# Performance work log

Hardware: AMD Instinct MI355X
Metric: run time of the kernel (lower is better)

## Reference

```python
import jax, jax.numpy as jnp
import numpy as np

A = 9  # len(scales) * len(ratios) anchor templates
DN = ('NHWC', 'HWIO', 'NHWC')


def _conv(x, w, b):
    y = jax.lax.conv_general_dilated(x, w, window_strides=(1, 1), padding='SAME',
                                     dimension_numbers=DN)
    return y + b


def setup_inputs() -> dict:
    key = jax.random.key(0)
    ks = jax.random.split(key, 9)
    s = 0.02  # weight init scale
    x = jax.random.normal(ks[0], (4, 128, 128, 512), jnp.float32)
    W1 = jax.random.normal(ks[1], (3, 3, 512, 256), jnp.float32) * s
    b1 = jnp.zeros((256,), jnp.float32)
    W2 = jax.random.normal(ks[2], (3, 3, 256, 256), jnp.float32) * s
    b2 = jnp.zeros((256,), jnp.float32)
    Wr = jax.random.normal(ks[3], (1, 1, 256, 4 * A), jnp.float32) * s
    br = jnp.zeros((4 * A,), jnp.float32)
    Wc = jax.random.normal(ks[4], (1, 1, 256, 2 * A), jnp.float32) * s
    bc = jnp.zeros((2 * A,), jnp.float32)
    return {'x': x, 'W1': W1, 'b1': b1, 'W2': W2, 'b2': b2,
            'Wr': Wr, 'br': br, 'Wc': Wc, 'bc': bc}


def reference(x, W1, b1, W2, b2, Wr, br, Wc, bc):
    h = jax.nn.relu(_conv(x, W1, b1))
    h = jax.nn.relu(_conv(h, W2, b2))
    B, H, W = h.shape[0], h.shape[1], h.shape[2]
    reg = _conv(h, Wr, br).reshape(B, H, W, A, 4)            # (B,H,W,A,4)
    cls = _conv(h, Wc, bc).reshape(B, H, W, A, 2)            # (B,H,W,A,2)
    cls = jax.nn.softmax(cls, axis=4)
    return jnp.concatenate((cls, reg), axis=4)               # (B,H,W,A,6)
```

## Files before the change

### kernel.cpp

```cpp
#include <hip/hip_runtime.h>


typedef float f32x4  __attribute__((ext_vector_type(4)));
typedef float f32x16 __attribute__((ext_vector_type(16)));
typedef short bf16x8 __attribute__((ext_vector_type(8)));

union U16x8 { uint4 v; unsigned short s[8]; };

__device__ __forceinline__ unsigned short f2bf(float f) {
  union { float f; unsigned int u; } v; v.f = f;
  unsigned int r = v.u + 0x7FFFu + ((v.u >> 16) & 1u);
  return (unsigned short)(r >> 16);
}

__global__ __launch_bounds__(256) void transpose_cvt(
    const float* __restrict__ src, unsigned short* __restrict__ dst,
    int K, int N) {
  __shared__ float t[32][33];
  const int tx = threadIdx.x, ty = threadIdx.y;
  const int k0 = blockIdx.x * 32, n0 = blockIdx.y * 32;
  const float* s = src + (size_t)blockIdx.z * K * N;
  unsigned short* d = dst + (size_t)blockIdx.z * N * K;
#pragma unroll
  for (int r = 0; r < 32; r += 8) {
    int k = k0 + ty + r, n = n0 + tx;
    t[ty + r][tx] = (k < K && n < N) ? s[(size_t)k * N + n] : 0.f;
  }
  __syncthreads();
#pragma unroll
  for (int r = 0; r < 32; r += 8) {
    int n = n0 + ty + r, k = k0 + tx;
    if (n < N && k < K) d[(size_t)n * K + k] = f2bf(t[tx][ty + r]);
  }
}

__global__ __launch_bounds__(256) void convert_x(
    const float* __restrict__ x, unsigned short* __restrict__ xp) {
  int idx = blockIdx.x * 256 + threadIdx.x;
  int g = idx & 63;
  int cell = idx >> 6;
  int xpix = cell % 130;
  int t = cell / 130;
  int ypix = t % 130;
  int b = t / 130;
  U16x8 u;
  if (xpix == 0 || xpix == 129 || ypix == 0 || ypix == 129) {
    u.v = make_uint4(0u, 0u, 0u, 0u);
  } else {
    const float* sp = x + ((size_t)((b * 128 + ypix - 1) * 128) + (xpix - 1)) * 512 + g * 8;
    float4 a = *(const float4*)sp;
    float4 c = *(const float4*)(sp + 4);
    u.s[0] = f2bf(a.x); u.s[1] = f2bf(a.y); u.s[2] = f2bf(a.z); u.s[3] = f2bf(a.w);
    u.s[4] = f2bf(c.x); u.s[5] = f2bf(c.y); u.s[6] = f2bf(c.z); u.s[7] = f2bf(c.w);
  }
  *(uint4*)(xp + (size_t)cell * 512 + g * 8) = u.v;
}

__global__ __launch_bounds__(256) void zero_h1_borders(unsigned short* __restrict__ h1p) {
  int idx = blockIdx.x * 256 + threadIdx.x;
  int g = idx & 31;
  int cell = idx >> 5;
  int xpix = cell % 130;
  int t = cell / 130;
  int ypix = t % 130;
  if (xpix == 0 || xpix == 129 || ypix == 0 || ypix == 129)
    *(uint4*)(h1p + (size_t)cell * 256 + g * 8) = make_uint4(0u, 0u, 0u, 0u);
}

template<int CIN, int MODE>
__global__ __launch_bounds__(256) void conv3x3(
    const unsigned short* __restrict__ Ap,
    const unsigned short* __restrict__ WT,
    const float* __restrict__ bias,
    unsigned short* __restrict__ out) {
  __shared__ __align__(16) unsigned short As[130][72];
  __shared__ __align__(16) unsigned short Bs[3][128][72];
  const int tid  = threadIdx.x;
  const int wave = tid >> 6, lane = tid & 63;
  const int wm = wave >> 1, wn = wave & 1;
  const int l31 = lane & 31, hi = lane >> 5;
  const int b = blockIdx.x >> 7, y = blockIdx.x & 127;
  const int nbase = blockIdx.y * 128;

  f32x16 acc[2][2] = {};

  for (int dy = 0; dy < 3; ++dy) {
    const unsigned short* Arow = Ap + ((size_t)(b * 130 + y + dy) * 130) * CIN;
    const unsigned short* Btap = WT + ((size_t)(dy * 3) * 256 + nbase) * CIN;
    for (int ci0 = 0; ci0 < CIN; ci0 += 64) {
      for (int s = tid; s < 1040; s += 256) {
        int row = s >> 3, seg = s & 7;
        *(uint4*)&As[row][seg * 8] =
            *(const uint4*)(Arow + (size_t)row * CIN + ci0 + seg * 8);
      }
#pragma unroll
      for (int t = 0; t < 12; ++t) {
        int s = t * 256 + tid;
        int dx = s >> 10, r = (s >> 3) & 127, seg = s & 7;
        *(uint4*)&Bs[dx][r][seg * 8] =
            *(const uint4*)(Btap + ((size_t)dx * 256 + r) * CIN + ci0 + seg * 8);
      }
      __syncthreads();
#pragma unroll
      for (int dx = 0; dx < 3; ++dx) {
#pragma unroll
        for (int ks = 0; ks < 4; ++ks) {
          bf16x8 af[2], bfr[2];
#pragma unroll
          for (int i = 0; i < 2; ++i)
            af[i] = *(const bf16x8*)&As[wm * 64 + i * 32 + l31 + dx][ks * 16 + hi * 8];
#pragma unroll
          for (int j = 0; j < 2; ++j)
            bfr[j] = *(const bf16x8*)&Bs[dx][wn * 64 + j * 32 + l31][ks * 16 + hi * 8];
#pragma unroll
          for (int i = 0; i < 2; ++i)
#pragma unroll
            for (int j = 0; j < 2; ++j)
              acc[i][j] = __builtin_amdgcn_mfma_f32_32x32x16_bf16(af[i], bfr[j], acc[i][j], 0, 0, 0);
        }
      }
      __syncthreads();
    }
  }

#pragma unroll
  for (int i = 0; i < 2; ++i) {
#pragma unroll
    for (int j = 0; j < 2; ++j) {
      int n = nbase + wn * 64 + j * 32 + l31;
      float bb = bias[n];
#pragma unroll
      for (int reg = 0; reg < 16; ++reg) {
        int m = wm * 64 + i * 32 + (reg & 3) + 8 * (reg >> 2) + 4 * hi;
        float v = fmaxf(acc[i][j][reg] + bb, 0.f);
        size_t off;
        if (MODE == 0)
          off = ((size_t)(b * 130 + y + 1) * 130 + (m + 1)) * 256 + n;
        else
          off = ((size_t)((b * 128 + y) * 128 + m)) * 256 + n;
        out[off] = f2bf(v);
      }
    }
  }
}

__global__ __launch_bounds__(256) void heads_kernel(
    const unsigned short* __restrict__ h2,
    const unsigned short* __restrict__ WhT,
    const float* __restrict__ br, const float* __restrict__ bc,
    float* __restrict__ out) {
  __shared__ __align__(16) unsigned short As[64][264];
  const int tid = threadIdx.x;
  const int wave = tid >> 6, lane = tid & 63;
  const int quad = lane >> 4, l16 = lane & 15;
  const int pix0 = blockIdx.x * 64;
#pragma unroll
  for (int r = 0; r < 8; ++r) {
    int s = r * 256 + tid;
    int row = s >> 5, seg = s & 31;
    *(uint4*)&As[row][seg * 8] =
        *(const uint4*)(h2 + (size_t)(pix0 + row) * 256 + seg * 8);
  }
  __syncthreads();
  f32x4 acc[4] = {};
#pragma unroll
  for (int ks = 0; ks < 8; ++ks) {
    bf16x8 af = *(const bf16x8*)&As[wave * 16 + l16][ks * 32 + quad * 8];
#pragma unroll
    for (int j = 0; j < 4; ++j) {
      bf16x8 bfr = *(const bf16x8*)(WhT + (size_t)(j * 16 + l16) * 256 + ks * 32 + quad * 8);
      acc[j] = __builtin_amdgcn_mfma_f32_16x16x32_bf16(af, bfr, acc[j], 0, 0, 0);
    }
  }
#pragma unroll
  for (int j = 0; j < 4; ++j) {
    int n = j * 16 + l16;
    float bias = 0.f;
    if (n < 18) bias = bc[n];
    else if (n < 54) bias = br[n - 18];
#pragma unroll
    for (int r = 0; r < 4; ++r) {
      int p = pix0 + wave * 16 + quad * 4 + r;
      float v = acc[j][r] + bias;
      float partner = __shfl_xor(v, 1);
      if (n < 18) {
        float mx = fmaxf(v, partner);
        float e0 = __expf(v - mx), e1 = __expf(partner - mx);
        int a = n >> 1, sl = n & 1;
        out[(size_t)p * 54 + a * 6 + sl] = e0 / (e0 + e1);
      } else if (n < 54) {
        int rr = n - 18, a = rr >> 2, sl = (rr & 3) + 2;
        out[(size_t)p * 54 + a * 6 + sl] = v;
      }
    }
  }
}

extern "C" void kernel_launch(void* const* d_in, const int* in_sizes, int n_in,
                              void* d_out, int out_size, void* d_ws, size_t ws_size,
                              hipStream_t stream) {
  const float* x  = (const float*)d_in[0];
  const float* W1 = (const float*)d_in[1];
  const float* b1 = (const float*)d_in[2];
  const float* W2 = (const float*)d_in[3];
  const float* b2 = (const float*)d_in[4];
  const float* Wr = (const float*)d_in[5];
  const float* br = (const float*)d_in[6];
  const float* Wc = (const float*)d_in[7];
  const float* bc = (const float*)d_in[8];
  float* out = (float*)d_out;

  constexpr size_t XPAD_B  = 4ull * 130 * 130 * 512 * 2;
  constexpr size_t H1PAD_B = 4ull * 130 * 130 * 256 * 2;
  constexpr size_t H2_B    = 4ull * 128 * 128 * 256 * 2;
  constexpr size_t W1T_B   = 9ull * 256 * 512 * 2;
  constexpr size_t W2T_B   = 9ull * 256 * 256 * 2;
  char* ws = (char*)d_ws;
  unsigned short* x_pad  = (unsigned short*)(ws);
  unsigned short* h1_pad = (unsigned short*)(ws + XPAD_B);
  unsigned short* h2     = (unsigned short*)(ws + XPAD_B + H1PAD_B);
  unsigned short* W1T    = (unsigned short*)(ws + XPAD_B + H1PAD_B + H2_B);
  unsigned short* W2T    = (unsigned short*)(ws + XPAD_B + H1PAD_B + H2_B + W1T_B);
  unsigned short* WhT    = (unsigned short*)(ws + XPAD_B + H1PAD_B + H2_B + W1T_B + W2T_B);

  hipMemsetAsync(WhT, 0, 64ull * 256 * 2, stream);
  transpose_cvt<<<dim3(16, 8, 9), dim3(32, 8), 0, stream>>>(W1, W1T, 512, 256);
  transpose_cvt<<<dim3(8, 8, 9),  dim3(32, 8), 0, stream>>>(W2, W2T, 256, 256);
  transpose_cvt<<<dim3(8, 1, 1),  dim3(32, 8), 0, stream>>>(Wc, WhT, 256, 18);
  transpose_cvt<<<dim3(8, 2, 1),  dim3(32, 8), 0, stream>>>(Wr, WhT + 18 * 256, 256, 36);
  convert_x<<<16900, 256, 0, stream>>>(x, x_pad);
  zero_h1_borders<<<8450, 256, 0, stream>>>(h1_pad);
  conv3x3<512, 0><<<dim3(512, 2), 256, 0, stream>>>(x_pad, W1T, b1, h1_pad);
  conv3x3<256, 1><<<dim3(512, 2), 256, 0, stream>>>(h1_pad, W2T, b2, h2);
  heads_kernel<<<1024, 256, 0, stream>>>(h2, WhT, br, bc, out);
}
```

Measured before the change: 511.7 us.

## Double-buffer conv tiles with direct global-to-LDS loads and XOR swizzle

The 3x3 conv kernel now stages its A and B tiles with global_load_lds into two LDS buffers. The next (dy, channel-chunk) slice is prefetched while MFMAs run on the current one, with an XOR swizzle in place of row padding to avoid bank conflicts. This aims to hide global load latency and remove the register round-trip and one barrier per iteration. LDS use doubles, to about 114KB per block, which may cut occupancy. Separately, the h1 border-zeroing kernel now launches only over border cells instead of scanning the whole padded tensor.

```diff
diff --git a/kernel.cpp b/kernel.cpp
--- a/kernel.cpp
+++ b/kernel.cpp
@@ -11,6 +11,12 @@
   union { float f; unsigned int u; } v; v.f = f;
   unsigned int r = v.u + 0x7FFFu + ((v.u >> 16) & 1u);
   return (unsigned short)(r >> 16);
+}
+
+__device__ __forceinline__ void cp16(const unsigned short* g, unsigned short* l) {
+  __builtin_amdgcn_global_load_lds(
+      (const __attribute__((address_space(1))) unsigned int*)g,
+      (__attribute__((address_space(3))) unsigned int*)l, 16, 0, 0);
 }
 
 __global__ __launch_bounds__(256) void transpose_cvt(
@@ -60,11 +66,13 @@
   int idx = blockIdx.x * 256 + threadIdx.x;
   int g = idx & 31;
   int cell = idx >> 5;
-  int xpix = cell % 130;
-  int t = cell / 130;
-  int ypix = t % 130;
-  if (xpix == 0 || xpix == 129 || ypix == 0 || ypix == 129)
-    *(uint4*)(h1p + (size_t)cell * 256 + g * 8) = make_uint4(0u, 0u, 0u, 0u);
+  int b = cell / 516, c = cell % 516;
+  int row, col;
+  if (c < 130)      { row = 0;   col = c; }
+  else if (c < 260) { row = 129; col = c - 130; }
+  else { int e = c - 260; row = 1 + (e >> 1); col = (e & 1) * 129; }
+  size_t ci = ((size_t)(b * 130) + row) * 130 + col;
+  *(uint4*)(h1p + ci * 256 + g * 8) = make_uint4(0u, 0u, 0u, 0u);
 }
 
 template<int CIN, int MODE>
@@ -73,54 +81,74 @@
     const unsigned short* __restrict__ WT,
     const float* __restrict__ bias,
     unsigned short* __restrict__ out) {
-  __shared__ __align__(16) unsigned short As[130][72];
-  __shared__ __align__(16) unsigned short Bs[3][128][72];
+  constexpr int NC = CIN / 64;
+  constexpr int NI = 3 * NC;
+  __shared__ __align__(16) unsigned short As[2][130 * 64];
+  __shared__ __align__(16) unsigned short Bs[2][3 * 128 * 64];
   const int tid  = threadIdx.x;
   const int wave = tid >> 6, lane = tid & 63;
   const int wm = wave >> 1, wn = wave & 1;
   const int l31 = lane & 31, hi = lane >> 5;
+  const int q  = lane >> 3;
+  const int sp = lane & 7;
+  const int sl = sp ^ q;
   const int b = blockIdx.x >> 7, y = blockIdx.x & 127;
   const int nbase = blockIdx.y * 128;
 
+  auto stage = [&](int buf, int it) {
+    int dy = it / NC, ci0 = (it - dy * NC) * 64;
+    const unsigned short* Arow = Ap + ((size_t)(b * 130 + y + dy) * 130) * CIN + ci0;
+    const unsigned short* Bt   = WT + ((size_t)(dy * 3) * 256 + nbase) * CIN + ci0;
+#pragma unroll
+    for (int c = wave; c < 16; c += 4) {
+      int r = c * 8 + q;
+      cp16(Arow + (size_t)r * CIN + sl * 8, &As[buf][c * 512 + lane * 8]);
+    }
+    if (wave == 0 && lane < 16) {
+      int r = 128 + q;
+      cp16(Arow + (size_t)r * CIN + sl * 8, &As[buf][16 * 512 + lane * 8]);
+    }
+#pragma unroll
+    for (int c = wave; c < 48; c += 4) {
+      int gi = c * 8 + q;
+      int dx = gi >> 7, rr = gi & 127;
+      cp16(Bt + ((size_t)dx * 256 + rr) * CIN + sl * 8, &Bs[buf][c * 512 + lane * 8]);
+    }
+  };
+
   f32x16 acc[2][2] = {};
 
-  for (int dy = 0; dy < 3; ++dy) {
-    const unsigned short* Arow = Ap + ((size_t)(b * 130 + y + dy) * 130) * CIN;
-    const unsigned short* Btap = WT + ((size_t)(dy * 3) * 256 + nbase) * CIN;
-    for (int ci0 = 0; ci0 < CIN; ci0 += 64) {
-      for (int s = tid; s < 1040; s += 256) {
-        int row = s >> 3, seg = s & 7;
-        *(uint4*)&As[row][seg * 8] =
-            *(const uint4*)(Arow + (size_t)row * CIN + ci0 + seg * 8);
+  stage(0, 0);
+  __syncthreads();
+  int cur = 0;
+  for (int it = 0; it < NI; ++it) {
+    if (it + 1 < NI) stage(cur ^ 1, it + 1);
+#pragma unroll
+    for (int dx = 0; dx < 3; ++dx) {
+#pragma unroll
+      for (int ks = 0; ks < 4; ++ks) {
+        bf16x8 af[2], bfr[2];
+#pragma unroll
+        for (int i = 0; i < 2; ++i) {
+          int row = wm * 64 + i * 32 + l31 + dx;
+          int sgp = (ks * 2 + hi) ^ (row & 7);
+          af[i] = *(const bf16x8*)&As[cur][row * 64 + sgp * 8];
+        }
+#pragma unroll
+        for (int j = 0; j < 2; ++j) {
+          int rw = wn * 64 + j * 32 + l31;
+          int sgp = (ks * 2 + hi) ^ (rw & 7);
+          bfr[j] = *(const bf16x8*)&Bs[cur][(dx * 128 + rw) * 64 + sgp * 8];
+        }
+#pragma unroll
+        for (int i = 0; i < 2; ++i)
+#pragma unroll
+          for (int j = 0; j < 2; ++j)
+            acc[i][j] = __builtin_amdgcn_mfma_f32_32x32x16_bf16(af[i], bfr[j], acc[i][j], 0, 0, 0);
       }
-#pragma unroll
-      for (int t = 0; t < 12; ++t) {
-        int s = t * 256 + tid;
-        int dx = s >> 10, r = (s >> 3) & 127, seg = s & 7;
-        *(uint4*)&Bs[dx][r][seg * 8] =
-            *(const uint4*)(Btap + ((size_t)dx * 256 + r) * CIN + ci0 + seg * 8);
-      }
-      __syncthreads();
-#pragma unroll
-      for (int dx = 0; dx < 3; ++dx) {
-#pragma unroll
-        for (int ks = 0; ks < 4; ++ks) {
-          bf16x8 af[2], bfr[2];
-#pragma unroll
-          for (int i = 0; i < 2; ++i)
-            af[i] = *(const bf16x8*)&As[wm * 64 + i * 32 + l31 + dx][ks * 16 + hi * 8];
-#pragma unroll
-          for (int j = 0; j < 2; ++j)
-            bfr[j] = *(const bf16x8*)&Bs[dx][wn * 64 + j * 32 + l31][ks * 16 + hi * 8];
-#pragma unroll
-          for (int i = 0; i < 2; ++i)
-#pragma unroll
-            for (int j = 0; j < 2; ++j)
-              acc[i][j] = __builtin_amdgcn_mfma_f32_32x32x16_bf16(af[i], bfr[j], acc[i][j], 0, 0, 0);
-        }
-      }
-      __syncthreads();
-    }
+    }
+    __syncthreads();
+    cur ^= 1;
   }
 
 #pragma unroll
@@ -186,11 +214,11 @@
       if (n < 18) {
         float mx = fmaxf(v, partner);
         float e0 = __expf(v - mx), e1 = __expf(partner - mx);
-        int a = n >> 1, sl = n & 1;
-        out[(size_t)p * 54 + a * 6 + sl] = e0 / (e0 + e1);
+        int a = n >> 1, sl2 = n & 1;
+        out[(size_t)p * 54 + a * 6 + sl2] = e0 / (e0 + e1);
       } else if (n < 54) {
-        int rr = n - 18, a = rr >> 2, sl = (rr & 3) + 2;
-        out[(size_t)p * 54 + a * 6 + sl] = v;
+        int rr = n - 18, a = rr >> 2, sl2 = (rr & 3) + 2;
+        out[(size_t)p * 54 + a * 6 + sl2] = v;
       }
     }
   }
@@ -229,7 +257,7 @@
   transpose_cvt<<<dim3(8, 1, 1),  dim3(32, 8), 0, stream>>>(Wc, WhT, 256, 18);
   transpose_cvt<<<dim3(8, 2, 1),  dim3(32, 8), 0, stream>>>(Wr, WhT + 18 * 256, 256, 36);
   convert_x<<<16900, 256, 0, stream>>>(x, x_pad);
-  zero_h1_borders<<<8450, 256, 0, stream>>>(h1_pad);
+  zero_h1_borders<<<258, 256, 0, stream>>>(h1_pad);
   conv3x3<512, 0><<<dim3(512, 2), 256, 0, stream>>>(x_pad, W1T, b1, h1_pad);
   conv3x3<256, 1><<<dim3(512, 2), 256, 0, stream>>>(h1_pad, W2T, b2, h2);
   heads_kernel<<<1024, 256, 0, stream>>>(h2, WhT, br, bc, out);
```

Result: slower. 590.2 us (+15.3%).
